# Performance work log

Hardware: AMD Instinct MI355X
Metric: run time of the kernel (lower is better)

## Reference

```python
import jax, jax.numpy as jnp
import numpy as np

N_NODES = 20000
DIM = 128
N_EDGES = 500000
BATCH = 16384
EPS = 1e-6  # torch.nn.PairwiseDistance default eps


def setup_inputs() -> dict:
    key = jax.random.key(0)
    k = jax.random.split(key, 8)
    edges = jax.random.randint(k[0], (2, N_EDGES), 0, N_NODES, dtype=jnp.int64 if jax.config.jax_enable_x64 else jnp.int32)
    nodes_p_star = jnp.sort(jax.random.randint(k[1], (BATCH,), 0, N_NODES))
    nodes_p = jnp.sort(jax.random.randint(k[2], (BATCH,), 0, N_NODES))
    # learned parameters, init in [-1, 1) as in the torch module
    beta_p = 2.0 * jax.random.uniform(k[3], (N_NODES,), dtype=jnp.float32) - 1.0
    beta_p_star = 2.0 * jax.random.uniform(k[4], (N_NODES,), dtype=jnp.float32) - 1.0
    p = 2.0 * jax.random.uniform(k[5], (N_NODES, DIM), dtype=jnp.float32) - 1.0
    p_star = 2.0 * jax.random.uniform(k[6], (N_NODES, DIM), dtype=jnp.float32) - 1.0
    return {
        "edges": edges,
        "nodes_p_star": nodes_p_star,
        "nodes_p": nodes_p,
        "beta_p": beta_p,
        "beta_p_star": beta_p_star,
        "p": p,
        "p_star": p_star,
    }


def reference(edges, nodes_p_star, nodes_p, beta_p, beta_p_star, p, p_star):
    # ---- link term: sum over observed edges of (beta - dist) ----
    beta_pair = beta_p_star[edges[0]] + beta_p[edges[1]]  # [E]
    diff = p[edges[0]] - p_star[edges[1]]                 # [E, D]
    # torch PairwiseDistance adds eps to the difference before the norm
    z_dist = jnp.sqrt(jnp.sum((diff + EPS) ** 2, axis=-1))
    link_term = jnp.sum(beta_pair - z_dist)

    # ---- non-link term: triu-masked sum of exp(beta - cdist) ----
    bps = beta_p_star[nodes_p_star]   # [Ns]
    bp = beta_p[nodes_p]              # [Np]
    ps = p_star[nodes_p_star]         # [Ns, D]
    pp = p[nodes_p]                   # [Np, D]
    beta_mat = bps[None, :] + bp[:, None]          # [Np, Ns]
    # cdist(ps, pp) -> [Ns, Np] via Gram trick
    sq = (jnp.sum(ps * ps, axis=-1)[:, None]
          + jnp.sum(pp * pp, axis=-1)[None, :]
          - 2.0 * jnp.einsum('nd,md->nm', ps, pp))
    dist_mat = jnp.sqrt(jnp.maximum(sq, 0.0))      # [Ns, Np]
    intensity = jnp.exp(beta_mat.T - dist_mat)     # [Ns, Np]
    non_link = jnp.sum(jnp.triu(intensity, k=1))

    return -(link_term - non_link)
```

## Files before the change

kernel.cpp:

```cpp
#include <hip/hip_runtime.h>
#include <hip/hip_bf16.h>

#define N_NODES 20000
#define DIM 128
#define N_EDGES 500000
#define BATCH 16384
#define EPS 1e-6f
#define L2E 1.4426950408889634f

typedef _Float16 half8 __attribute__((ext_vector_type(8)));
typedef _Float16 half4_t __attribute__((ext_vector_type(4)));
typedef float f32x4 __attribute__((ext_vector_type(4)));

__device__ __forceinline__ float fast_sqrtf(float x) {
#if __has_builtin(__builtin_amdgcn_sqrtf)
    return __builtin_amdgcn_sqrtf(x);
#else
    return sqrtf(x);
#endif
}
__device__ __forceinline__ float fast_exp2f(float x) {
#if __has_builtin(__builtin_amdgcn_exp2f)
    return __builtin_amdgcn_exp2f(x);
#else
    return exp2f(x);
#endif
}

#define OFF_PSH   33280
#define OFF_PPH   4227584
#define OFF_N2S   8421888
#define OFF_N2P   8487424
#define OFF_BPS   8552960
#define OFF_BP    8618496
#define OFF_P16   8684032
#define OFF_PS16  13804032
#define OFF_END   18924032

__global__ __launch_bounds__(256) void prep_kernel(
    const float* __restrict__ p, const float* __restrict__ p_star,
    const float* __restrict__ beta_p, const float* __restrict__ beta_ps,
    const int* __restrict__ nodes_ps, const int* __restrict__ nodes_p,
    _Float16* __restrict__ Ah, float* __restrict__ n2A, float* __restrict__ bA2,
    _Float16* __restrict__ Bh, float* __restrict__ n2B, float* __restrict__ bB2,
    _Float16* __restrict__ p16, _Float16* __restrict__ ps16, int use16,
    float* __restrict__ out)
{
    const int bx = blockIdx.x;
    if (bx == 0 && threadIdx.x == 0) out[0] = 0.f;
    if (bx < 4096) {
        const int g = threadIdx.x & 31;
        const int r8 = threadIdx.x >> 5;
        const bool isA = bx < 2048;
        int row = (isA ? bx : bx - 2048) * 8 + r8;
        int id = isA ? nodes_ps[row] : nodes_p[row];
        const float* src = isA ? p_star : p;
        float4 v = ((const float4*)(src + (size_t)id * DIM))[g];
        half4_t o;
        o[0] = (_Float16)v.x; o[1] = (_Float16)v.y; o[2] = (_Float16)v.z; o[3] = (_Float16)v.w;
        _Float16* dst = isA ? Ah : Bh;
        *(half4_t*)(dst + (size_t)row * DIM + g * 4) = o;
        float nrm = v.x * v.x + v.y * v.y + v.z * v.z + v.w * v.w;
        #pragma unroll
        for (int m = 16; m >= 1; m >>= 1) nrm += __shfl_xor(nrm, m, 32);
        if (g == 0) {
            if (isA) { n2A[row] = nrm; bA2[row] = L2E * beta_ps[id]; }
            else     { n2B[row] = nrm; bB2[row] = L2E * beta_p[id]; }
        }
    } else if (use16) {
        int b = bx - 4096;
        const bool isP = b < 1250;
        const float* src = isP ? p : p_star;
        _Float16* dst = isP ? p16 : ps16;
        int base = (isP ? b : b - 1250) * 512 + threadIdx.x;
        #pragma unroll
        for (int u = 0; u < 2; ++u) {
            int f4 = base + u * 256;
            float4 v = ((const float4*)src)[f4];
            half4_t o;
            o[0] = (_Float16)v.x; o[1] = (_Float16)v.y; o[2] = (_Float16)v.z; o[3] = (_Float16)v.w;
            ((half4_t*)dst)[f4] = o;
        }
    }
}

__global__ __launch_bounds__(512, 4) void main_kernel(
    const _Float16* __restrict__ Ag, const _Float16* __restrict__ Bg,
    const float* __restrict__ n2A, const float* __restrict__ n2B,
    const float* __restrict__ bA2, const float* __restrict__ bB2,
    const int* __restrict__ edges,
    const float* __restrict__ beta_p, const float* __restrict__ beta_ps,
    const _Float16* __restrict__ p16, const _Float16* __restrict__ ps16,
    const float* __restrict__ pf, const float* __restrict__ psf, int use16,
    float* __restrict__ out)
{
    const int bx = blockIdx.x, by = blockIdx.y;
    int ti, tj;
    const int len = 128 - by;
    if (bx < len) { ti = by; tj = by + bx; }
    else          { ti = 127 - by; tj = 127 - (bx - len); }
    const int i0 = ti * 128, j0 = tj * 128;
    const int bid = by * 129 + bx;
    const bool diag = (ti == tj);

    __shared__ __align__(16) _Float16 As[128][72];
    __shared__ __align__(16) _Float16 Bs[128][72];
    __shared__ float smr[8];

    const int tid = threadIdx.x;
    const int lane = tid & 63;
    const int w = tid >> 6;
    const int wm = w & 3;
    const int wn = w >> 2;
    const int quad = lane >> 4;
    const int lr = lane & 15;

    float lsum = 0.f;
    half8 ea[2], eb[2];
    float ebeta[2] = {0.f, 0.f};
    bool ev[2];
    #pragma unroll
    for (int t = 0; t < 2; ++t) {
        int e = bid * 64 + w * 8 + quad * 2 + t;
        ev[t] = (e < N_EDGES);
        if (ev[t]) {
            int e0 = edges[e];
            int e1 = edges[N_EDGES + e];
            if (use16) {
                ea[t] = *(const half8*)(p16 + (size_t)e0 * DIM + lr * 8);
                eb[t] = *(const half8*)(ps16 + (size_t)e1 * DIM + lr * 8);
                if (lr == 0) ebeta[t] = beta_ps[e0] + beta_p[e1];
            } else {
                const float* ar = pf + (size_t)e0 * DIM + lr * 8;
                const float* br = psf + (size_t)e1 * DIM + lr * 8;
                float s = 0.f;
                #pragma unroll
                for (int k = 0; k < 8; ++k) {
                    float d = ar[k] - br[k] + EPS;
                    s = fmaf(d, d, s);
                }
                #pragma unroll
                for (int m = 8; m >= 1; m >>= 1) s += __shfl_xor(s, m, 16);
                if (lr == 0) lsum -= (beta_ps[e0] + beta_p[e1]) - fast_sqrtf(s);
            }
        }
    }

    const int ilo = i0 + wm * 32, jlo = j0 + wn * 64;
    float4 n2i[2], bi[2];
    #pragma unroll
    for (int mi = 0; mi < 2; ++mi) {
        n2i[mi] = *(const float4*)&n2A[ilo + mi * 16 + quad * 4];
        bi[mi]  = *(const float4*)&bA2[ilo + mi * 16 + quad * 4];
    }
    float n2j[4], bj[4];
    #pragma unroll
    for (int ni = 0; ni < 4; ++ni) {
        n2j[ni] = n2B[jlo + ni * 16 + lr];
        bj[ni]  = bB2[jlo + ni * 16 + lr];
    }

    int cls = 0;
    if (diag) cls = (wn == 0) ? (wm >= 2 ? 2 : 1) : (wm >= 2 ? 1 : 0);

    f32x4 acc[2][4] = {};
    #pragma unroll
    for (int kh = 0; kh < 2; ++kh) {
        if (kh) __syncthreads();
        #pragma unroll
        for (int c = tid; c < 1024; c += 512) {
            int row = c >> 3, col = (c & 7) * 8;
            *(uint4*)&As[row][col] = *(const uint4*)(Ag + (size_t)(i0 + row) * DIM + kh * 64 + col);
            *(uint4*)&Bs[row][col] = *(const uint4*)(Bg + (size_t)(j0 + row) * DIM + kh * 64 + col);
        }
        __syncthreads();
        if (cls != 2) {
            #pragma unroll
            for (int ks = 0; ks < 2; ++ks) {
                int koff = ks * 32 + quad * 8;
                half8 af[2], bf[4];
                #pragma unroll
                for (int u = 0; u < 2; ++u) af[u] = *(const half8*)&As[wm * 32 + u * 16 + lr][koff];
                #pragma unroll
                for (int v = 0; v < 4; ++v) bf[v] = *(const half8*)&Bs[wn * 64 + v * 16 + lr][koff];
                #pragma unroll
                for (int mi = 0; mi < 2; ++mi)
                    #pragma unroll
                    for (int ni = 0; ni < 4; ++ni)
                        acc[mi][ni] = __builtin_amdgcn_mfma_f32_16x16x32_f16(af[mi], bf[ni], acc[mi][ni], 0, 0, 0);
            }
        }
    }

    if (cls != 2) {
        if (cls == 0) {
            #pragma unroll
            for (int mi = 0; mi < 2; ++mi)
                #pragma unroll
                for (int ni = 0; ni < 4; ++ni) {
                    f32x4 d = acc[mi][ni];
                    #pragma unroll
                    for (int r = 0; r < 4; ++r) {
                        float tt = ((const float*)&n2i[mi])[r] + n2j[ni];
                        float sq = fmaxf(fmaf(d[r], -2.f, tt), 0.f);
                        float arg = fmaf(fast_sqrtf(sq), -L2E, ((const float*)&bi[mi])[r] + bj[ni]);
                        lsum += fast_exp2f(arg);
                    }
                }
        } else {
            #pragma unroll
            for (int mi = 0; mi < 2; ++mi)
                #pragma unroll
                for (int ni = 0; ni < 4; ++ni) {
                    f32x4 d = acc[mi][ni];
                    #pragma unroll
                    for (int r = 0; r < 4; ++r) {
                        int ig = ilo + mi * 16 + quad * 4 + r;
                        int jg = jlo + ni * 16 + lr;
                        float tt = ((const float*)&n2i[mi])[r] + n2j[ni];
                        float sq = fmaxf(fmaf(d[r], -2.f, tt), 0.f);
                        float arg = fmaf(fast_sqrtf(sq), -L2E, ((const float*)&bi[mi])[r] + bj[ni]);
                        float ex = fast_exp2f(arg);
                        if (jg > ig) lsum += ex;
                    }
                }
        }
    }

    if (use16) {
        #pragma unroll
        for (int t = 0; t < 2; ++t) {
            if (ev[t]) {
                float s = 0.f;
                #pragma unroll
                for (int k = 0; k < 8; ++k) {
                    float d = (float)ea[t][k] - (float)eb[t][k] + EPS;
                    s = fmaf(d, d, s);
                }
                #pragma unroll
                for (int m = 8; m >= 1; m >>= 1) s += __shfl_xor(s, m, 16);
                if (lr == 0) lsum -= ebeta[t] - fast_sqrtf(s);
            }
        }
    }

    #pragma unroll
    for (int m = 32; m >= 1; m >>= 1) lsum += __shfl_xor(lsum, m, 64);
    if (lane == 0) smr[w] = lsum;
    __syncthreads();
    if (tid == 0) {
        float t = 0.f;
        #pragma unroll
        for (int i = 0; i < 8; ++i) t += smr[i];
        atomicAdd(out, t);
    }
}

extern "C" void kernel_launch(void* const* d_in, const int* in_sizes, int n_in,
                              void* d_out, int out_size, void* d_ws, size_t ws_size,
                              hipStream_t stream) {
    const int* edges = (const int*)d_in[0];
    const int* nodes_p_star = (const int*)d_in[1];
    const int* nodes_p = (const int*)d_in[2];
    const float* beta_p = (const float*)d_in[3];
    const float* beta_p_star = (const float*)d_in[4];
    const float* p = (const float*)d_in[5];
    const float* p_star = (const float*)d_in[6];

    char* ws = (char*)d_ws;
    _Float16* psh = (_Float16*)(ws + OFF_PSH);
    _Float16* pph = (_Float16*)(ws + OFF_PPH);
    float* n2s = (float*)(ws + OFF_N2S);
    float* n2p = (float*)(ws + OFF_N2P);
    float* bps2 = (float*)(ws + OFF_BPS);
    float* bp2 = (float*)(ws + OFF_BP);
    _Float16* p16 = (_Float16*)(ws + OFF_P16);
    _Float16* ps16 = (_Float16*)(ws + OFF_PS16);

    const int use16 = (ws_size >= (size_t)OFF_END) ? 1 : 0;

    prep_kernel<<<6596, 256, 0, stream>>>(
        p, p_star, beta_p, beta_p_star, nodes_p_star, nodes_p,
        psh, n2s, bps2, pph, n2p, bp2, p16, ps16, use16, (float*)d_out);

    main_kernel<<<dim3(129, 64), 512, 0, stream>>>(
        psh, pph, n2s, n2p, bps2, bp2,
        edges, beta_p, beta_p_star, p16, ps16, p, p_star, use16,
        (float*)d_out);
}
```

Measured before the change: 226.8 us.

## Switch Gram matrix and edge gathers from fp16 to fp8 e4m3 with single-stage LDS load

After: 197.3 us. 1.15x faster.

```diff
diff --git a/kernel.cpp b/kernel.cpp
--- a/kernel.cpp
+++ b/kernel.cpp
@@ -1,5 +1,6 @@
 #include <hip/hip_runtime.h>
 #include <hip/hip_bf16.h>
+#include <hip/hip_fp8.h>
 
 #define N_NODES 20000
 #define DIM 128
@@ -8,9 +9,9 @@
 #define EPS 1e-6f
 #define L2E 1.4426950408889634f
 
-typedef _Float16 half8 __attribute__((ext_vector_type(8)));
-typedef _Float16 half4_t __attribute__((ext_vector_type(4)));
 typedef float f32x4 __attribute__((ext_vector_type(4)));
+typedef float f32x2 __attribute__((ext_vector_type(2)));
+typedef long long i64_t;
 
 __device__ __forceinline__ float fast_sqrtf(float x) {
 #if __has_builtin(__builtin_amdgcn_sqrtf)
@@ -27,23 +28,49 @@
 #endif
 }
 
-#define OFF_PSH   33280
-#define OFF_PPH   4227584
-#define OFF_N2S   8421888
-#define OFF_N2P   8487424
-#define OFF_BPS   8552960
-#define OFF_BP    8618496
-#define OFF_P16   8684032
-#define OFF_PS16  13804032
-#define OFF_END   18924032
+__device__ __forceinline__ unsigned pack4_fp8(float a, float b, float c, float d) {
+#if __has_builtin(__builtin_amdgcn_cvt_pk_fp8_f32)
+    unsigned v = 0;
+    v = __builtin_amdgcn_cvt_pk_fp8_f32(a, b, v, false);
+    v = __builtin_amdgcn_cvt_pk_fp8_f32(c, d, v, true);
+    return v;
+#else
+    __hip_fp8_e4m3 x0(a), x1(b), x2(c), x3(d);
+    return (unsigned)x0.__x | ((unsigned)x1.__x << 8) |
+           ((unsigned)x2.__x << 16) | ((unsigned)x3.__x << 24);
+#endif
+}
+
+template <bool HI>
+__device__ __forceinline__ f32x2 unpack2_fp8(unsigned v) {
+#if __has_builtin(__builtin_amdgcn_cvt_pk_f32_fp8)
+    return __builtin_amdgcn_cvt_pk_f32_fp8((int)v, HI);
+#else
+    __hip_fp8_e4m3 t0, t1;
+    t0.__x = (unsigned char)(HI ? (v >> 16) : v);
+    t1.__x = (unsigned char)(HI ? (v >> 24) : (v >> 8));
+    f32x2 r; r.x = (float)t0; r.y = (float)t1;
+    return r;
+#endif
+}
+
+#define OFF_A8   0
+#define OFF_B8   2097152
+#define OFF_N2S  4194304
+#define OFF_N2P  4259840
+#define OFF_BPS  4325376
+#define OFF_BP   4390912
+#define OFF_P8   4456448
+#define OFF_PS8  7016448
+#define OFF_END  9576448
 
 __global__ __launch_bounds__(256) void prep_kernel(
     const float* __restrict__ p, const float* __restrict__ p_star,
     const float* __restrict__ beta_p, const float* __restrict__ beta_ps,
     const int* __restrict__ nodes_ps, const int* __restrict__ nodes_p,
-    _Float16* __restrict__ Ah, float* __restrict__ n2A, float* __restrict__ bA2,
-    _Float16* __restrict__ Bh, float* __restrict__ n2B, float* __restrict__ bB2,
-    _Float16* __restrict__ p16, _Float16* __restrict__ ps16, int use16,
+    unsigned char* __restrict__ A8, float* __restrict__ n2A, float* __restrict__ bA2,
+    unsigned char* __restrict__ B8, float* __restrict__ n2B, float* __restrict__ bB2,
+    unsigned char* __restrict__ p8, unsigned char* __restrict__ ps8,
     float* __restrict__ out)
 {
     const int bx = blockIdx.x;
@@ -56,10 +83,9 @@
         int id = isA ? nodes_ps[row] : nodes_p[row];
         const float* src = isA ? p_star : p;
         float4 v = ((const float4*)(src + (size_t)id * DIM))[g];
-        half4_t o;
-        o[0] = (_Float16)v.x; o[1] = (_Float16)v.y; o[2] = (_Float16)v.z; o[3] = (_Float16)v.w;
-        _Float16* dst = isA ? Ah : Bh;
-        *(half4_t*)(dst + (size_t)row * DIM + g * 4) = o;
+        unsigned pk = pack4_fp8(v.x, v.y, v.z, v.w);
+        unsigned char* dst = isA ? A8 : B8;
+        ((unsigned*)(dst + (size_t)row * DIM))[g] = pk;
         float nrm = v.x * v.x + v.y * v.y + v.z * v.z + v.w * v.w;
         #pragma unroll
         for (int m = 16; m >= 1; m >>= 1) nrm += __shfl_xor(nrm, m, 32);
@@ -67,31 +93,29 @@
             if (isA) { n2A[row] = nrm; bA2[row] = L2E * beta_ps[id]; }
             else     { n2B[row] = nrm; bB2[row] = L2E * beta_p[id]; }
         }
-    } else if (use16) {
+    } else {
         int b = bx - 4096;
         const bool isP = b < 1250;
         const float* src = isP ? p : p_star;
-        _Float16* dst = isP ? p16 : ps16;
+        unsigned char* dst = isP ? p8 : ps8;
         int base = (isP ? b : b - 1250) * 512 + threadIdx.x;
         #pragma unroll
         for (int u = 0; u < 2; ++u) {
             int f4 = base + u * 256;
             float4 v = ((const float4*)src)[f4];
-            half4_t o;
-            o[0] = (_Float16)v.x; o[1] = (_Float16)v.y; o[2] = (_Float16)v.z; o[3] = (_Float16)v.w;
-            ((half4_t*)dst)[f4] = o;
-        }
-    }
-}
-
+            ((unsigned*)dst)[f4] = pack4_fp8(v.x, v.y, v.z, v.w);
+        }
+    }
+}
+
+#define LSTRIDE 144
 __global__ __launch_bounds__(512, 4) void main_kernel(
-    const _Float16* __restrict__ Ag, const _Float16* __restrict__ Bg,
+    const unsigned char* __restrict__ Ag, const unsigned char* __restrict__ Bg,
     const float* __restrict__ n2A, const float* __restrict__ n2B,
     const float* __restrict__ bA2, const float* __restrict__ bB2,
     const int* __restrict__ edges,
     const float* __restrict__ beta_p, const float* __restrict__ beta_ps,
-    const _Float16* __restrict__ p16, const _Float16* __restrict__ ps16,
-    const float* __restrict__ pf, const float* __restrict__ psf, int use16,
+    const unsigned char* __restrict__ p8, const unsigned char* __restrict__ ps8,
     float* __restrict__ out)
 {
     const int bx = blockIdx.x, by = blockIdx.y;
@@ -103,8 +127,8 @@
     const int bid = by * 129 + bx;
     const bool diag = (ti == tj);
 
-    __shared__ __align__(16) _Float16 As[128][72];
-    __shared__ __align__(16) _Float16 Bs[128][72];
+    __shared__ __align__(16) unsigned char As[128 * LSTRIDE];
+    __shared__ __align__(16) unsigned char Bs[128 * LSTRIDE];
     __shared__ float smr[8];
 
     const int tid = threadIdx.x;
@@ -116,34 +140,17 @@
     const int lr = lane & 15;
 
     float lsum = 0.f;
-    half8 ea[2], eb[2];
-    float ebeta[2] = {0.f, 0.f};
-    bool ev[2];
-    #pragma unroll
-    for (int t = 0; t < 2; ++t) {
-        int e = bid * 64 + w * 8 + quad * 2 + t;
-        ev[t] = (e < N_EDGES);
-        if (ev[t]) {
-            int e0 = edges[e];
-            int e1 = edges[N_EDGES + e];
-            if (use16) {
-                ea[t] = *(const half8*)(p16 + (size_t)e0 * DIM + lr * 8);
-                eb[t] = *(const half8*)(ps16 + (size_t)e1 * DIM + lr * 8);
-                if (lr == 0) ebeta[t] = beta_ps[e0] + beta_p[e1];
-            } else {
-                const float* ar = pf + (size_t)e0 * DIM + lr * 8;
-                const float* br = psf + (size_t)e1 * DIM + lr * 8;
-                float s = 0.f;
-                #pragma unroll
-                for (int k = 0; k < 8; ++k) {
-                    float d = ar[k] - br[k] + EPS;
-                    s = fmaf(d, d, s);
-                }
-                #pragma unroll
-                for (int m = 8; m >= 1; m >>= 1) s += __shfl_xor(s, m, 16);
-                if (lr == 0) lsum -= (beta_ps[e0] + beta_p[e1]) - fast_sqrtf(s);
-            }
-        }
+    const int le = bid * 64 + w * 8 + (lane >> 3);
+    const int lch = lane & 7;
+    const bool ev = (le < N_EDGES);
+    uint4 ua, ub;
+    float ebeta = 0.f;
+    if (ev) {
+        int e0 = edges[le];
+        int e1 = edges[N_EDGES + le];
+        ua = *(const uint4*)(p8 + (size_t)e0 * DIM + lch * 16);
+        ub = *(const uint4*)(ps8 + (size_t)e1 * DIM + lch * 16);
+        if (lch == 0) ebeta = beta_ps[e0] + beta_p[e1];
     }
 
     const int ilo = i0 + wm * 32, jlo = j0 + wn * 64;
@@ -160,39 +167,36 @@
         bj[ni]  = bB2[jlo + ni * 16 + lr];
     }
 
+    #pragma unroll
+    for (int c = tid; c < 1024; c += 512) {
+        int row = c >> 3, col = (c & 7) * 16;
+        *(uint4*)&As[row * LSTRIDE + col] = *(const uint4*)(Ag + (size_t)(i0 + row) * DIM + col);
+        *(uint4*)&Bs[row * LSTRIDE + col] = *(const uint4*)(Bg + (size_t)(j0 + row) * DIM + col);
+    }
+    __syncthreads();
+
     int cls = 0;
     if (diag) cls = (wn == 0) ? (wm >= 2 ? 2 : 1) : (wm >= 2 ? 1 : 0);
 
-    f32x4 acc[2][4] = {};
-    #pragma unroll
-    for (int kh = 0; kh < 2; ++kh) {
-        if (kh) __syncthreads();
-        #pragma unroll
-        for (int c = tid; c < 1024; c += 512) {
-            int row = c >> 3, col = (c & 7) * 8;
-            *(uint4*)&As[row][col] = *(const uint4*)(Ag + (size_t)(i0 + row) * DIM + kh * 64 + col);
-            *(uint4*)&Bs[row][col] = *(const uint4*)(Bg + (size_t)(j0 + row) * DIM + kh * 64 + col);
-        }
-        __syncthreads();
-        if (cls != 2) {
-            #pragma unroll
-            for (int ks = 0; ks < 2; ++ks) {
-                int koff = ks * 32 + quad * 8;
-                half8 af[2], bf[4];
+    if (cls != 2) {
+        f32x4 acc[2][4] = {};
+        #pragma unroll
+        for (int ks = 0; ks < 4; ++ks) {
+            int koff = ks * 32 + quad * 8;
+            i64_t af[2], bf[4];
+            #pragma unroll
+            for (int u = 0; u < 2; ++u)
+                af[u] = *(const i64_t*)&As[(wm * 32 + u * 16 + lr) * LSTRIDE + koff];
+            #pragma unroll
+            for (int v = 0; v < 4; ++v)
+                bf[v] = *(const i64_t*)&Bs[(wn * 64 + v * 16 + lr) * LSTRIDE + koff];
+            #pragma unroll
+            for (int mi = 0; mi < 2; ++mi)
                 #pragma unroll
-                for (int u = 0; u < 2; ++u) af[u] = *(const half8*)&As[wm * 32 + u * 16 + lr][koff];
-                #pragma unroll
-                for (int v = 0; v < 4; ++v) bf[v] = *(const half8*)&Bs[wn * 64 + v * 16 + lr][koff];
-                #pragma unroll
-                for (int mi = 0; mi < 2; ++mi)
-                    #pragma unroll
-                    for (int ni = 0; ni < 4; ++ni)
-                        acc[mi][ni] = __builtin_amdgcn_mfma_f32_16x16x32_f16(af[mi], bf[ni], acc[mi][ni], 0, 0, 0);
-            }
-        }
-    }
-
-    if (cls != 2) {
+                for (int ni = 0; ni < 4; ++ni)
+                    acc[mi][ni] = __builtin_amdgcn_mfma_f32_16x16x32_fp8_fp8(af[mi], bf[ni], acc[mi][ni], 0, 0, 0);
+        }
+
         if (cls == 0) {
             #pragma unroll
             for (int mi = 0; mi < 2; ++mi)
@@ -227,21 +231,22 @@
         }
     }
 
-    if (use16) {
-        #pragma unroll
-        for (int t = 0; t < 2; ++t) {
-            if (ev[t]) {
-                float s = 0.f;
-                #pragma unroll
-                for (int k = 0; k < 8; ++k) {
-                    float d = (float)ea[t][k] - (float)eb[t][k] + EPS;
-                    s = fmaf(d, d, s);
-                }
-                #pragma unroll
-                for (int m = 8; m >= 1; m >>= 1) s += __shfl_xor(s, m, 16);
-                if (lr == 0) lsum -= ebeta[t] - fast_sqrtf(s);
-            }
-        }
+    if (ev) {
+        float s = 0.f;
+        #pragma unroll
+        for (int d = 0; d < 4; ++d) {
+            unsigned va = ((const unsigned*)&ua)[d];
+            unsigned vb = ((const unsigned*)&ub)[d];
+            f32x2 a0 = unpack2_fp8<false>(va), a1 = unpack2_fp8<true>(va);
+            f32x2 b0 = unpack2_fp8<false>(vb), b1 = unpack2_fp8<true>(vb);
+            float t0 = a0.x - b0.x + EPS, t1 = a0.y - b0.y + EPS;
+            float t2 = a1.x - b1.x + EPS, t3 = a1.y - b1.y + EPS;
+            s = fmaf(t0, t0, s); s = fmaf(t1, t1, s);
+            s = fmaf(t2, t2, s); s = fmaf(t3, t3, s);
+        }
+        #pragma unroll
+        for (int m = 4; m >= 1; m >>= 1) s += __shfl_xor(s, m, 8);
+        if (lch == 0) lsum -= ebeta - fast_sqrtf(s);
     }
 
     #pragma unroll
@@ -268,23 +273,20 @@
     const float* p_star = (const float*)d_in[6];
 
     char* ws = (char*)d_ws;
-    _Float16* psh = (_Float16*)(ws + OFF_PSH);
-    _Float16* pph = (_Float16*)(ws + OFF_PPH);
+    unsigned char* A8 = (unsigned char*)(ws + OFF_A8);
+    unsigned char* B8 = (unsigned char*)(ws + OFF_B8);
     float* n2s = (float*)(ws + OFF_N2S);
     float* n2p = (float*)(ws + OFF_N2P);
     float* bps2 = (float*)(ws + OFF_BPS);
     float* bp2 = (float*)(ws + OFF_BP);
-    _Float16* p16 = (_Float16*)(ws + OFF_P16);
-    _Float16* ps16 = (_Float16*)(ws + OFF_PS16);
-
-    const int use16 = (ws_size >= (size_t)OFF_END) ? 1 : 0;
+    unsigned char* p8 = (unsigned char*)(ws + OFF_P8);
+    unsigned char* ps8 = (unsigned char*)(ws + OFF_PS8);
 
     prep_kernel<<<6596, 256, 0, stream>>>(
         p, p_star, beta_p, beta_p_star, nodes_p_star, nodes_p,
-        psh, n2s, bps2, pph, n2p, bp2, p16, ps16, use16, (float*)d_out);
+        A8, n2s, bps2, B8, n2p, bp2, p8, ps8, (float*)d_out);
 
     main_kernel<<<dim3(129, 64), 512, 0, stream>>>(
-        psh, pph, n2s, n2p, bps2, bp2,
-        edges, beta_p, beta_p_star, p16, ps16, p, p_star, use16,
-        (float*)d_out);
-}
+        A8, B8, n2s, n2p, bps2, bp2,
+        edges, beta_p, beta_p_star, p8, ps8, (float*)d_out);
+}
```
